# Optimization experiments

Hardware: AMD Instinct MI355X
Metric: run time of the kernel (lower is better)

The kernel has to match this reference:

```python
import jax, jax.numpy as jnp
import numpy as np
from jax import lax
from jax.scipy.special import logsumexp

B, S, T = 64, 512, 32
END_IND = T - 1  # module-level global in the original repo; bind to last tag


def setup_inputs() -> dict:
    key = jax.random.key(0)
    k1, k2, k3 = jax.random.split(key, 3)
    scores = jax.random.normal(k1, (B, S, T, T), dtype=jnp.float32)
    targets = jax.random.randint(k2, (B, S), 0, T * T, dtype=jnp.int32).astype(jnp.int64)
    # lengths in [1, S], sorted descending (pack_padded_sequence assumption)
    lengths = jnp.sort(jax.random.randint(k3, (B,), 1, S + 1, dtype=jnp.int32))[::-1]
    return {"scores": scores, "targets": targets, "lengths": lengths}


def reference(scores, targets, lengths):
    Bs, Ss, Ts, _ = scores.shape
    # gold score: gather flattened tag-pair score at each valid timestep
    flat = scores.reshape(Bs, Ss, Ts * Ts)
    gathered = jnp.take_along_axis(flat, targets[..., None], axis=2)[..., 0]  # [B,S]
    time_mask = jnp.arange(Ss)[None, :] < lengths[:, None]  # [B,S]
    gold_score = jnp.sum(jnp.where(time_mask, gathered, 0.0))

    # forward algorithm: fs[b, cur_tag], recurrence lse over prev_tag
    fs0 = logsumexp(scores[:, 0], axis=2)  # [B,T]
    sc_rest = jnp.swapaxes(scores, 0, 1)[1:]  # [S-1, B, T, T]
    active = jnp.arange(1, Ss)[:, None] < lengths[None, :]  # [S-1, B]

    def step(fs, xs):
        sc_t, act = xs  # [B,T,T], [B]
        new = logsumexp(sc_t + fs[:, None, :], axis=2)  # [B,T]
        return jnp.where(act[:, None], new, fs), None

    fs, _ = lax.scan(step, fs0, (sc_rest, active))
    all_scores = jnp.sum(fs[:, END_IND])
    return all_scores - gold_score
```

## Files before the change

### kernel.cpp

```cpp
#include <hip/hip_runtime.h>
#include <hip/hip_bf16.h>

#define BB 64
#define SS 512
#define TT 32
#define ENDI 31
#define ACCS 0
#define CNTS 1
#define GOLDB 16

typedef __attribute__((ext_vector_type(8))) short s8v;
typedef __attribute__((ext_vector_type(16))) float fx16;

union S8U {
  s8v v;
  unsigned int u[4];
};

__device__ __forceinline__ unsigned int cvtpk_bf16(float a, float b) {
  unsigned int r;
  asm("v_cvt_pk_bf16_f32 %0, %1, %2" : "=v"(r) : "v"(a), "v"(b));
  return r;
}

__global__ __launch_bounds__(64) void seg_kernel(
    const float* __restrict__ sc, const int* __restrict__ targets,
    const int* __restrict__ lengths, float* __restrict__ ws, int nseg,
    int seglen) {
  const int b = blockIdx.x;
  const int seg = blockIdx.y;
  const int l = threadIdx.x;
  const int c = l & 31;
  const int h = l >> 5;
  const int len = lengths[b];
  const int lo = seg * seglen;

  if (b == 0 && seg == 0 && l == 0) {
    ws[ACCS] = 0.0f;
    ((unsigned*)ws)[CNTS] = 0u;
  }

  {
    float gv = 0.f;
    for (int s0 = l; s0 < seglen; s0 += 64) {
      int s = lo + s0;
      if (s < len) {
        int idx = b * SS + s;
        gv += sc[(size_t)idx * 1024 + (size_t)targets[idx]];
      }
    }
#pragma unroll
    for (int o = 32; o; o >>= 1) gv += __shfl_xor(gv, o);
    if (l == 0) ws[GOLDB + b * nseg + seg] = gv;
  }

  float* mout = ws + GOLDB + BB * nseg + (size_t)(b * nseg + seg) * 1056;

  if (len <= lo) {
#pragma unroll
    for (int r = 0; r < 16; ++r) {
      int row = (r & 3) + 8 * (r >> 2) + 4 * h;
      mout[row * 32 + c] = (row == c) ? 1.0f : 0.0f;
    }
    if (l == 0) mout[1024] = 0.0f;
    return;
  }

  const int hi = (lo + seglen < len) ? (lo + seglen) : len;
  const int nsteps = hi - lo;
  const float* base = sc + ((size_t)b * SS + lo) * 1024;

  S8U B0, B1;
#pragma unroll
  for (int q = 0; q < 4; ++q) {
    B0.u[q] = 0u;
    B1.u[q] = 0u;
  }
  {
    int j0 = c - 8 * h;
    if (j0 >= 0 && j0 < 8) B0.u[j0 >> 1] |= 0x3F80u << (16 * (j0 & 1));
    int j1 = c - 16 - 8 * h;
    if (j1 >= 0 && j1 < 8) B1.u[j1 >> 1] |= 0x3F80u << (16 * (j1 & 1));
  }

#define LOADE(buf, T)                                                     \
  do {                                                                    \
    const float* _p = base + (size_t)(T) * 1024 + c * 32 + 8 * h;         \
    float4 _a = *(const float4*)_p;                                       \
    float4 _b = *(const float4*)(_p + 4);                                 \
    float4 _c = *(const float4*)(_p + 16);                                \
    float4 _d = *(const float4*)(_p + 20);                                \
    buf[0] = _a.x;  buf[1] = _a.y;  buf[2] = _a.z;  buf[3] = _a.w;        \
    buf[4] = _b.x;  buf[5] = _b.y;  buf[6] = _b.z;  buf[7] = _b.w;        \
    buf[8] = _c.x;  buf[9] = _c.y;  buf[10] = _c.z; buf[11] = _c.w;       \
    buf[12] = _d.x; buf[13] = _d.y; buf[14] = _d.z; buf[15] = _d.w;       \
  } while (0)

#define STEPB(RB)                                                            \
  do {                                                                      \
    S8U A0, A1;                                                             \
    _Pragma("unroll") for (int q = 0; q < 4; ++q) {                         \
      A0.u[q] = cvtpk_bf16(__expf(RB[2 * q]), __expf(RB[2 * q + 1]));       \
      A1.u[q] = cvtpk_bf16(__expf(RB[8 + 2 * q]), __expf(RB[9 + 2 * q]));   \
    }                                                                       \
    int _pf = t + 3;                                                        \
    if (_pf >= nsteps) _pf = nsteps - 1;                                    \
    LOADE(RB, _pf);                                                         \
    fx16 Cl;                                                                \
    _Pragma("unroll") for (int q = 0; q < 16; ++q) Cl[q] = 0.f;             \
    Cl = __builtin_amdgcn_mfma_f32_32x32x16_bf16(A0.v, B0.v, Cl, 0, 0, 0);  \
    Cl = __builtin_amdgcn_mfma_f32_32x32x16_bf16(A1.v, B1.v, Cl, 0, 0, 0);  \
    if (t + 1 < nsteps) {                                                   \
      float _s = 1.0f;                                                      \
      if ((t & 3) == 3) {              \
        float _mx = Cl[0];                                                  \
        _Pragma("unroll") for (int q = 1; q < 16; ++q) _mx =                \
            fmaxf(_mx, Cl[q]);                                              \
        _mx = fmaxf(_mx, __shfl_xor(_mx, 32));                              \
        _mx = fmaxf(_mx, __shfl_xor(_mx, 1));                               \
        _mx = fmaxf(_mx, __shfl_xor(_mx, 2));                               \
        _mx = fmaxf(_mx, __shfl_xor(_mx, 4));                               \
        _mx = fmaxf(_mx, __shfl_xor(_mx, 8));                               \
        _mx = fmaxf(_mx, __shfl_xor(_mx, 16));                              \
        int _ex = ((__float_as_int(_mx) >> 23) & 255) - 127;                \
        _s = __int_as_float((unsigned)(127 - _ex) << 23);                   \
        esum += _ex;                                                        \
      }                                                                     \
      unsigned int W[8], X[8];                                              \
      _Pragma("unroll") for (int q = 0; q < 8; ++q) W[q] =                  \
          cvtpk_bf16(Cl[2 * q] * _s, Cl[2 * q + 1] * _s);                   \
      _Pragma("unroll") for (int q = 0; q < 8; ++q) X[q] =                  \
          __shfl_xor((int)W[q], 32);                                        \
      B0.u[0] = h ? X[2] : W[0];                                            \
      B0.u[1] = h ? X[3] : W[1];                                            \
      B0.u[2] = h ? W[2] : X[0];                                            \
      B0.u[3] = h ? W[3] : X[1];                                            \
      B1.u[0] = h ? X[6] : W[4];                                            \
      B1.u[1] = h ? X[7] : W[5];                                            \
      B1.u[2] = h ? W[6] : X[4];                                            \
      B1.u[3] = h ? W[7] : X[5];                                            \
    } else {                                                                \
      C = Cl;                                                               \
    }                                                                       \
  } while (0)

  float r0[16], r1[16], r2[16];
  LOADE(r0, 0);
  LOADE(r1, (nsteps > 1) ? 1 : 0);
  LOADE(r2, (nsteps > 2) ? 2 : 0);
  int esum = 0;
  fx16 C;
#pragma unroll
  for (int q = 0; q < 16; ++q) C[q] = 0.f;

  int t = 0;
  while (t < nsteps) {
    STEPB(r0);
    ++t;
    if (t >= nsteps) break;
    STEPB(r1);
    ++t;
    if (t >= nsteps) break;
    STEPB(r2);
    ++t;
  }

  float mx = C[0];
#pragma unroll
  for (int q = 1; q < 16; ++q) mx = fmaxf(mx, C[q]);
  mx = fmaxf(mx, __shfl_xor(mx, 32));
  mx = fmaxf(mx, __shfl_xor(mx, 1));
  mx = fmaxf(mx, __shfl_xor(mx, 2));
  mx = fmaxf(mx, __shfl_xor(mx, 4));
  mx = fmaxf(mx, __shfl_xor(mx, 8));
  mx = fmaxf(mx, __shfl_xor(mx, 16));
  int ex = ((__float_as_int(mx) >> 23) & 255) - 127;
  float s = __int_as_float((unsigned)(127 - ex) << 23);
  esum += ex;
#pragma unroll
  for (int r = 0; r < 16; ++r) {
    int row = (r & 3) + 8 * (r >> 2) + 4 * h;
    mout[row * 32 + c] = C[r] * s;
  }
  if (l == 0) mout[1024] = (float)esum;
#undef STEPB
#undef LOADE
}

__global__ __launch_bounds__(128) void comb_fin_kernel(
    float* __restrict__ ws, int nseg, float* __restrict__ out) {
  const int b = blockIdx.x;
  const int w = threadIdx.x >> 6;
  const int l = threadIdx.x & 63;
  const int lo = l & 31;
  const int h = l >> 5;
  const int half = nseg >> 1;
  __shared__ alignas(16) float st[2][TT];
  __shared__ float esvS[2];

#define FENCE() asm volatile("s_waitcnt lgkmcnt(0)" ::: "memory")

  float cur = w ? ((lo == ENDI) ? 1.0f : 0.0f) : 1.0f;
  st[w][lo] = cur;
  FENCE();

  const float* segbase = ws + GOLDB + BB * nseg;
  float esv = 0.f;

#define LOADM(buf, SEG)                                                     \
  do {                                                                      \
    const float* _m = segbase + (size_t)(b * nseg + (SEG)) * 1056;          \
    if (w == 0) {                        \
      const float4* _p = (const float4*)(_m + lo * 32 + h * 16);            \
      float4 _a = _p[0], _b2 = _p[1], _c2 = _p[2], _d = _p[3];              \
      buf[0] = _a.x;  buf[1] = _a.y;  buf[2] = _a.z;  buf[3] = _a.w;        \
      buf[4] = _b2.x; buf[5] = _b2.y; buf[6] = _b2.z; buf[7] = _b2.w;       \
      buf[8] = _c2.x; buf[9] = _c2.y; buf[10] = _c2.z; buf[11] = _c2.w;     \
      buf[12] = _d.x; buf[13] = _d.y; buf[14] = _d.z; buf[15] = _d.w;       \
    } else {                              \
      const float* _p = _m + (h * 16) * 32 + lo;                            \
      _Pragma("unroll") for (int _j = 0; _j < 16; ++_j)                     \
          buf[_j] = _p[_j * 32];                                            \
    }                                                                       \
  } while (0)

  float mc[16], mn[16];
#pragma unroll
  for (int q = 0; q < 16; ++q) mn[q] = 0.f;
  {
    int seg0 = w ? (nseg - 1) : 0;
    LOADM(mc, seg0);
  }
  for (int k = 0; k < half; ++k) {
    int segn = w ? (nseg - 2 - k) : (k + 1);
    if (k + 1 < half) LOADM(mn, segn);
    int segc = w ? (nseg - 1 - k) : k;
    esv += segbase[(size_t)(b * nseg + segc) * 1056 + 1024];
    const float4* g4 = (const float4*)st[w];
    float4 g0 = g4[h * 4 + 0], g1 = g4[h * 4 + 1], g2 = g4[h * 4 + 2],
           g3 = g4[h * 4 + 3];
    float g[16] = {g0.x, g0.y, g0.z, g0.w, g1.x, g1.y, g1.z, g1.w,
                   g2.x, g2.y, g2.z, g2.w, g3.x, g3.y, g3.z, g3.w};
    float acc[4];
#pragma unroll
    for (int q = 0; q < 4; ++q) {
      acc[q] = mc[4 * q] * g[4 * q];
#pragma unroll
      for (int t = 1; t < 4; ++t)
        acc[q] = fmaf(mc[4 * q + t], g[4 * q + t], acc[q]);
    }
    float part = (acc[0] + acc[1]) + (acc[2] + acc[3]);
    cur = part + __shfl_xor(part, 32);
    if ((k & 3) == 3) {
      float mxv = cur;
      mxv = fmaxf(mxv, __shfl_xor(mxv, 1));
      mxv = fmaxf(mxv, __shfl_xor(mxv, 2));
      mxv = fmaxf(mxv, __shfl_xor(mxv, 4));
      mxv = fmaxf(mxv, __shfl_xor(mxv, 8));
      mxv = fmaxf(mxv, __shfl_xor(mxv, 16));
      int exv = ((__float_as_int(mxv) >> 23) & 255) - 127;
      cur *= __int_as_float((unsigned)(127 - exv) << 23);
      esv += (float)exv;
    }
    FENCE();
    st[w][lo] = cur;
    FENCE();
#pragma unroll
    for (int q = 0; q < 16; ++q) mc[q] = mn[q];
  }

  if (l == 0) esvS[w] = esv;
  __syncthreads();

  if (w == 0) {
    float pr = st[0][lo] * st[1][lo];
    float gd = (lo < nseg) ? ws[GOLDB + b * nseg + lo] : 0.f;
#pragma unroll
    for (int o = 16; o; o >>= 1) {
      pr += __shfl_xor(pr, o);
      gd += __shfl_xor(gd, o);
    }
    if (l == 0) {
      float loss =
          (esvS[0] + esvS[1]) * 0.6931471805599453f + __logf(pr) - gd;
      atomicAdd(&ws[ACCS], loss);
      __threadfence();
      unsigned old = atomicAdd(&((unsigned*)ws)[CNTS], 1u);
      if (old == BB - 1) {
        float v = atomicAdd(&ws[ACCS], 0.0f);
        out[0] = v;
      }
    }
  }
#undef LOADM
#undef FENCE
}

extern "C" void kernel_launch(void* const* d_in, const int* in_sizes, int n_in,
                              void* d_out, int out_size, void* d_ws,
                              size_t ws_size, hipStream_t stream) {
  const float* scores = (const float*)d_in[0];
  const int* targets = (const int*)d_in[1];
  const int* lengths = (const int*)d_in[2];
  float* out = (float*)d_out;
  float* ws = (float*)d_ws;

  int nseg = 32;
  while (nseg > 2) {
    size_t need =
        (size_t)(GOLDB + BB * nseg + (size_t)BB * nseg * 1056) * sizeof(float);
    if (need <= ws_size) break;
    nseg >>= 1;
  }
  int seglen = SS / nseg;

  seg_kernel<<<dim3(BB, nseg), 64, 0, stream>>>(scores, targets, lengths, ws,
                                                nseg, seglen);
  comb_fin_kernel<<<BB, 128, 0, stream>>>(ws, nseg, out);
}
```

Baseline: 51.24 us.

## Hardcode 32 segments and batch full-segment steps in chunks of four

Fixes the segment count and segment length at compile time, which removes the runtime workspace-size fallback and simplifies indexing. For full 16-step segments it adds a specialised path that loads four timesteps at once, computes their exponentials and bf16 packing together, and prefetches the next chunk of four before running the dependent MFMA chain. This aims to hide global load latency and the transcendental work behind the serial matrix recurrence. It raises register pressure, and it assumes the workspace is always large enough for 32 segments.

```diff
diff --git a/kernel.cpp b/kernel.cpp
--- a/kernel.cpp
+++ b/kernel.cpp
@@ -5,6 +5,8 @@
 #define SS 512
 #define TT 32
 #define ENDI 31
+#define NSEG 32
+#define SEGLEN 16
 #define ACCS 0
 #define CNTS 1
 #define GOLDB 16
@@ -25,15 +27,14 @@
 
 __global__ __launch_bounds__(64) void seg_kernel(
     const float* __restrict__ sc, const int* __restrict__ targets,
-    const int* __restrict__ lengths, float* __restrict__ ws, int nseg,
-    int seglen) {
+    const int* __restrict__ lengths, float* __restrict__ ws) {
   const int b = blockIdx.x;
   const int seg = blockIdx.y;
   const int l = threadIdx.x;
   const int c = l & 31;
   const int h = l >> 5;
   const int len = lengths[b];
-  const int lo = seg * seglen;
+  const int lo = seg * SEGLEN;
 
   if (b == 0 && seg == 0 && l == 0) {
     ws[ACCS] = 0.0f;
@@ -42,19 +43,19 @@
 
   {
     float gv = 0.f;
-    for (int s0 = l; s0 < seglen; s0 += 64) {
-      int s = lo + s0;
+    if (l < SEGLEN) {
+      int s = lo + l;
       if (s < len) {
         int idx = b * SS + s;
-        gv += sc[(size_t)idx * 1024 + (size_t)targets[idx]];
+        gv = sc[(size_t)idx * 1024 + (size_t)targets[idx]];
       }
     }
 #pragma unroll
     for (int o = 32; o; o >>= 1) gv += __shfl_xor(gv, o);
-    if (l == 0) ws[GOLDB + b * nseg + seg] = gv;
-  }
-
-  float* mout = ws + GOLDB + BB * nseg + (size_t)(b * nseg + seg) * 1056;
+    if (l == 0) ws[GOLDB + b * NSEG + seg] = gv;
+  }
+
+  float* mout = ws + GOLDB + BB * NSEG + (size_t)(b * NSEG + seg) * 1056;
 
   if (len <= lo) {
 #pragma unroll
@@ -66,8 +67,7 @@
     return;
   }
 
-  const int hi = (lo + seglen < len) ? (lo + seglen) : len;
-  const int nsteps = hi - lo;
+  const int nsteps = (len - lo < SEGLEN) ? (len - lo) : SEGLEN;
   const float* base = sc + ((size_t)b * SS + lo) * 1024;
 
   S8U B0, B1;
@@ -96,73 +96,124 @@
     buf[12] = _d.x; buf[13] = _d.y; buf[14] = _d.z; buf[15] = _d.w;       \
   } while (0)
 
-#define STEPB(RB)                                                            \
-  do {                                                                      \
-    S8U A0, A1;                                                             \
-    _Pragma("unroll") for (int q = 0; q < 4; ++q) {                         \
-      A0.u[q] = cvtpk_bf16(__expf(RB[2 * q]), __expf(RB[2 * q + 1]));       \
-      A1.u[q] = cvtpk_bf16(__expf(RB[8 + 2 * q]), __expf(RB[9 + 2 * q]));   \
-    }                                                                       \
-    int _pf = t + 3;                                                        \
-    if (_pf >= nsteps) _pf = nsteps - 1;                                    \
-    LOADE(RB, _pf);                                                         \
-    fx16 Cl;                                                                \
-    _Pragma("unroll") for (int q = 0; q < 16; ++q) Cl[q] = 0.f;             \
-    Cl = __builtin_amdgcn_mfma_f32_32x32x16_bf16(A0.v, B0.v, Cl, 0, 0, 0);  \
-    Cl = __builtin_amdgcn_mfma_f32_32x32x16_bf16(A1.v, B1.v, Cl, 0, 0, 0);  \
-    if (t + 1 < nsteps) {                                                   \
-      float _s = 1.0f;                                                      \
-      if ((t & 3) == 3) {              \
-        float _mx = Cl[0];                                                  \
-        _Pragma("unroll") for (int q = 1; q < 16; ++q) _mx =                \
-            fmaxf(_mx, Cl[q]);                                              \
-        _mx = fmaxf(_mx, __shfl_xor(_mx, 32));                              \
-        _mx = fmaxf(_mx, __shfl_xor(_mx, 1));                               \
-        _mx = fmaxf(_mx, __shfl_xor(_mx, 2));                               \
-        _mx = fmaxf(_mx, __shfl_xor(_mx, 4));                               \
-        _mx = fmaxf(_mx, __shfl_xor(_mx, 8));                               \
-        _mx = fmaxf(_mx, __shfl_xor(_mx, 16));                              \
-        int _ex = ((__float_as_int(_mx) >> 23) & 255) - 127;                \
-        _s = __int_as_float((unsigned)(127 - _ex) << 23);                   \
-        esum += _ex;                                                        \
-      }                                                                     \
-      unsigned int W[8], X[8];                                              \
-      _Pragma("unroll") for (int q = 0; q < 8; ++q) W[q] =                  \
-          cvtpk_bf16(Cl[2 * q] * _s, Cl[2 * q + 1] * _s);                   \
-      _Pragma("unroll") for (int q = 0; q < 8; ++q) X[q] =                  \
-          __shfl_xor((int)W[q], 32);                                        \
-      B0.u[0] = h ? X[2] : W[0];                                            \
-      B0.u[1] = h ? X[3] : W[1];                                            \
-      B0.u[2] = h ? W[2] : X[0];                                            \
-      B0.u[3] = h ? W[3] : X[1];                                            \
-      B1.u[0] = h ? X[6] : W[4];                                            \
-      B1.u[1] = h ? X[7] : W[5];                                            \
-      B1.u[2] = h ? W[6] : X[4];                                            \
-      B1.u[3] = h ? W[7] : X[5];                                            \
-    } else {                                                                \
-      C = Cl;                                                               \
-    }                                                                       \
+#define RESCALE(SVAR)                                                     \
+  do {                                                                    \
+    float _mx = Cl[0];                                                    \
+    _Pragma("unroll") for (int q = 1; q < 16; ++q) _mx = fmaxf(_mx, Cl[q]); \
+    _mx = fmaxf(_mx, __shfl_xor(_mx, 32));                                \
+    _mx = fmaxf(_mx, __shfl_xor(_mx, 1));                                 \
+    _mx = fmaxf(_mx, __shfl_xor(_mx, 2));                                 \
+    _mx = fmaxf(_mx, __shfl_xor(_mx, 4));                                 \
+    _mx = fmaxf(_mx, __shfl_xor(_mx, 8));                                 \
+    _mx = fmaxf(_mx, __shfl_xor(_mx, 16));                                \
+    int _ex = ((__float_as_int(_mx) >> 23) & 255) - 127;                  \
+    SVAR = __int_as_float((unsigned)(127 - _ex) << 23);                   \
+    esum += _ex;                                                          \
   } while (0)
 
-  float r0[16], r1[16], r2[16];
-  LOADE(r0, 0);
-  LOADE(r1, (nsteps > 1) ? 1 : 0);
-  LOADE(r2, (nsteps > 2) ? 2 : 0);
+#define REPACK()                                                          \
+  do {                                                                    \
+    unsigned int W[8], X[8];                                              \
+    _Pragma("unroll") for (int q = 0; q < 8; ++q) W[q] =                  \
+        cvtpk_bf16(Cl[2 * q] * s, Cl[2 * q + 1] * s);                     \
+    _Pragma("unroll") for (int q = 0; q < 8; ++q) X[q] =                  \
+        __shfl_xor((int)W[q], 32);                                        \
+    B0.u[0] = h ? X[2] : W[0];                                            \
+    B0.u[1] = h ? X[3] : W[1];                                            \
+    B0.u[2] = h ? W[2] : X[0];                                            \
+    B0.u[3] = h ? W[3] : X[1];                                            \
+    B1.u[0] = h ? X[6] : W[4];                                            \
+    B1.u[1] = h ? X[7] : W[5];                                            \
+    B1.u[2] = h ? W[6] : X[4];                                            \
+    B1.u[3] = h ? W[7] : X[5];                                            \
+  } while (0)
+
   int esum = 0;
   fx16 C;
 #pragma unroll
   for (int q = 0; q < 16; ++q) C[q] = 0.f;
 
-  int t = 0;
-  while (t < nsteps) {
-    STEPB(r0);
-    ++t;
-    if (t >= nsteps) break;
-    STEPB(r1);
-    ++t;
-    if (t >= nsteps) break;
-    STEPB(r2);
-    ++t;
+  if (nsteps == SEGLEN) {
+    float L[4][16];
+    S8U A4[4][2];
+#pragma unroll
+    for (int j = 0; j < 4; ++j) LOADE(L[j], j);
+
+#pragma unroll
+    for (int ch = 0; ch < 4; ++ch) {
+#pragma unroll
+      for (int k = 0; k < 4; ++k) {
+#pragma unroll
+        for (int q = 0; q < 4; ++q) {
+          A4[k][0].u[q] =
+              cvtpk_bf16(__expf(L[k][2 * q]), __expf(L[k][2 * q + 1]));
+          A4[k][1].u[q] =
+              cvtpk_bf16(__expf(L[k][8 + 2 * q]), __expf(L[k][9 + 2 * q]));
+        }
+      }
+      if (ch < 3) {
+#pragma unroll
+        for (int j = 0; j < 4; ++j) LOADE(L[j], (ch + 1) * 4 + j);
+      }
+#pragma unroll
+      for (int k = 0; k < 4; ++k) {
+        fx16 Cl;
+#pragma unroll
+        for (int q = 0; q < 16; ++q) Cl[q] = 0.f;
+        Cl = __builtin_amdgcn_mfma_f32_32x32x16_bf16(A4[k][0].v, B0.v, Cl,
+                                                     0, 0, 0);
+        Cl = __builtin_amdgcn_mfma_f32_32x32x16_bf16(A4[k][1].v, B1.v, Cl,
+                                                     0, 0, 0);
+        if (ch == 3 && k == 3) {
+          C = Cl;
+        } else {
+          float s = 1.0f;
+          if (k == 3) RESCALE(s);
+          REPACK();
+        }
+      }
+    }
+  } else {
+    float r0[16], r1[16], r2[16];
+    LOADE(r0, 0);
+    LOADE(r1, (nsteps > 1) ? 1 : 0);
+    LOADE(r2, (nsteps > 2) ? 2 : 0);
+
+#define STEPB(RB)                                                            \
+    do {                                                                    \
+      S8U A0, A1;                                                           \
+      _Pragma("unroll") for (int q = 0; q < 4; ++q) {                       \
+        A0.u[q] = cvtpk_bf16(__expf(RB[2 * q]), __expf(RB[2 * q + 1]));     \
+        A1.u[q] = cvtpk_bf16(__expf(RB[8 + 2 * q]), __expf(RB[9 + 2 * q])); \
+      }                                                                     \
+      int _pf = t + 3;                                                      \
+      if (_pf >= nsteps) _pf = nsteps - 1;                                  \
+      LOADE(RB, _pf);                                                       \
+      fx16 Cl;                                                              \
+      _Pragma("unroll") for (int q = 0; q < 16; ++q) Cl[q] = 0.f;           \
+      Cl = __builtin_amdgcn_mfma_f32_32x32x16_bf16(A0.v, B0.v, Cl, 0, 0, 0);\
+      Cl = __builtin_amdgcn_mfma_f32_32x32x16_bf16(A1.v, B1.v, Cl, 0, 0, 0);\
+      if (t + 1 < nsteps) {                                                 \
+        float s = 1.0f;                                                     \
+        if ((t & 3) == 3) RESCALE(s);                                       \
+        REPACK();                                                           \
+      } else {                                                              \
+        C = Cl;                                                             \
+      }                                                                     \
+    } while (0)
+
+    int t = 0;
+    while (t < nsteps) {
+      STEPB(r0);
+      ++t;
+      if (t >= nsteps) break;
+      STEPB(r1);
+      ++t;
+      if (t >= nsteps) break;
+      STEPB(r2);
+      ++t;
+    }
+#undef STEPB
   }
 
   float mx = C[0];
@@ -183,18 +234,19 @@
     mout[row * 32 + c] = C[r] * s;
   }
   if (l == 0) mout[1024] = (float)esum;
-#undef STEPB
+#undef REPACK
+#undef RESCALE
 #undef LOADE
 }
 
 __global__ __launch_bounds__(128) void comb_fin_kernel(
-    float* __restrict__ ws, int nseg, float* __restrict__ out) {
+    float* __restrict__ ws, float* __restrict__ out) {
   const int b = blockIdx.x;
   const int w = threadIdx.x >> 6;
   const int l = threadIdx.x & 63;
   const int lo = l & 31;
   const int h = l >> 5;
-  const int half = nseg >> 1;
+  const int half = NSEG >> 1;
   __shared__ alignas(16) float st[2][TT];
   __shared__ float esvS[2];
 
@@ -204,12 +256,12 @@
   st[w][lo] = cur;
   FENCE();
 
-  const float* segbase = ws + GOLDB + BB * nseg;
+  const float* segbase = ws + GOLDB + BB * NSEG;
   float esv = 0.f;
 
 #define LOADM(buf, SEG)                                                     \
   do {                                                                      \
-    const float* _m = segbase + (size_t)(b * nseg + (SEG)) * 1056;          \
+    const float* _m = segbase + (size_t)(b * NSEG + (SEG)) * 1056;          \
     if (w == 0) {                        \
       const float4* _p = (const float4*)(_m + lo * 32 + h * 16);            \
       float4 _a = _p[0], _b2 = _p[1], _c2 = _p[2], _d = _p[3];              \
@@ -217,7 +269,7 @@
       buf[4] = _b2.x; buf[5] = _b2.y; buf[6] = _b2.z; buf[7] = _b2.w;       \
       buf[8] = _c2.x; buf[9] = _c2.y; buf[10] = _c2.z; buf[11] = _c2.w;     \
       buf[12] = _d.x; buf[13] = _d.y; buf[14] = _d.z; buf[15] = _d.w;       \
-    } else {                              \
+    } else {      \
       const float* _p = _m + (h * 16) * 32 + lo;                            \
       _Pragma("unroll") for (int _j = 0; _j < 16; ++_j)                     \
           buf[_j] = _p[_j * 32];                                            \
@@ -228,14 +280,14 @@
 #pragma unroll
   for (int q = 0; q < 16; ++q) mn[q] = 0.f;
   {
-    int seg0 = w ? (nseg - 1) : 0;
+    int seg0 = w ? (NSEG - 1) : 0;
     LOADM(mc, seg0);
   }
   for (int k = 0; k < half; ++k) {
-    int segn = w ? (nseg - 2 - k) : (k + 1);
+    int segn = w ? (NSEG - 2 - k) : (k + 1);
     if (k + 1 < half) LOADM(mn, segn);
-    int segc = w ? (nseg - 1 - k) : k;
-    esv += segbase[(size_t)(b * nseg + segc) * 1056 + 1024];
+    int segc = w ? (NSEG - 1 - k) : k;
+    esv += segbase[(size_t)(b * NSEG + segc) * 1056 + 1024];
     const float4* g4 = (const float4*)st[w];
     float4 g0 = g4[h * 4 + 0], g1 = g4[h * 4 + 1], g2 = g4[h * 4 + 2],
            g3 = g4[h * 4 + 3];
@@ -274,7 +326,7 @@
 
   if (w == 0) {
     float pr = st[0][lo] * st[1][lo];
-    float gd = (lo < nseg) ? ws[GOLDB + b * nseg + lo] : 0.f;
+    float gd = ws[GOLDB + b * NSEG + lo];
 #pragma unroll
     for (int o = 16; o; o >>= 1) {
       pr += __shfl_xor(pr, o);
@@ -305,16 +357,6 @@
   float* out = (float*)d_out;
   float* ws = (float*)d_ws;
 
-  int nseg = 32;
-  while (nseg > 2) {
-    size_t need =
-        (size_t)(GOLDB + BB * nseg + (size_t)BB * nseg * 1056) * sizeof(float);
-    if (need <= ws_size) break;
-    nseg >>= 1;
-  }
-  int seglen = SS / nseg;
-
-  seg_kernel<<<dim3(BB, nseg), 64, 0, stream>>>(scores, targets, lengths, ws,
-                                                nseg, seglen);
-  comb_fin_kernel<<<BB, 128, 0, stream>>>(ws, nseg, out);
+  seg_kernel<<<dim3(BB, NSEG), 64, 0, stream>>>(scores, targets, lengths, ws);
+  comb_fin_kernel<<<BB, 128, 0, stream>>>(ws, out);
 }
```

New measurement: 49.79 us. -2.8%, faster.
